# Optimization experiments

Hardware: AMD Instinct MI355X
Metric: run time of the kernel (lower is better)

The kernel has to match this reference:

```python
import jax, jax.numpy as jnp
import numpy as np

V = 50257   # vocab size (output_size / num_words)
H = 500     # hidden_size
S = 256     # source sequence length
MAXLEN = 64 # greedy decode steps
SOS = 1


def _gru_scan(xs, Wih, Whh, bih, bhh, reverse=False):
    """Run a GRU over xs: (S, Din) -> (outputs (S,H), final hidden (H,)).
    PyTorch gate order: r, z, n."""
    gx = xs @ Wih.T + bih  # (S, 3H), input-side gates precomputed
    Hh = Whh.shape[1]
    h0 = jnp.zeros((Hh,), dtype=xs.dtype)

    def step(h, g):
        gh = Whh @ h + bhh
        rx, zx, nx = jnp.split(g, 3)
        rh, zh, nh = jnp.split(gh, 3)
        r = jax.nn.sigmoid(rx + rh)
        z = jax.nn.sigmoid(zx + zh)
        n = jnp.tanh(nx + r * nh)
        h2 = (1.0 - z) * n + z * h
        return h2, h2

    hT, ys = jax.lax.scan(step, h0, gx, reverse=reverse)
    return ys, hT


def _gru_cell(x, h, Wih, Whh, bih, bhh):
    gx = Wih @ x + bih
    gh = Whh @ h + bhh
    rx, zx, nx = jnp.split(gx, 3)
    rh, zh, nh = jnp.split(gh, 3)
    r = jax.nn.sigmoid(rx + rh)
    z = jax.nn.sigmoid(zx + zh)
    n = jnp.tanh(nx + r * nh)
    return (1.0 - z) * n + z * h


def setup_inputs() -> dict:
    key = jax.random.key(0)
    ks = jax.random.split(key, 32)

    def p(k, shape):
        return jax.random.normal(k, shape, dtype=jnp.float32) * 0.05

    inp = {}
    inp["input_seq"] = jax.random.randint(ks[0], (S, 1), 0, V)
    inp["input_length"] = S
    inp["max_length"] = MAXLEN
    inp["emb"] = p(ks[1], (V, H))
    i = 2
    for name, din in [("enc0f", H), ("enc0b", H), ("enc1f", 2 * H), ("enc1b", 2 * H)]:
        inp[name + "_Wih"] = p(ks[i], (3 * H, din)); i += 1
        inp[name + "_Whh"] = p(ks[i], (3 * H, H)); i += 1
        inp[name + "_bih"] = p(ks[i], (3 * H,)); i += 1
        inp[name + "_bhh"] = p(ks[i], (3 * H,)); i += 1
    inp["dec_Wih"] = p(ks[i], (2, 3 * H, H)); i += 1
    inp["dec_Whh"] = p(ks[i], (2, 3 * H, H)); i += 1
    inp["dec_bih"] = p(ks[i], (2, 3 * H)); i += 1
    inp["dec_bhh"] = p(ks[i], (2, 3 * H)); i += 1
    inp["concat_W"] = p(ks[i], (H, 2 * H)); i += 1
    inp["concat_b"] = p(ks[i], (H,)); i += 1
    inp["out_W"] = p(ks[i], (V, H)); i += 1
    inp["out_b"] = p(ks[i], (V,)); i += 1
    return inp


def reference(input_seq, input_length, max_length, emb,
              enc0f_Wih, enc0f_Whh, enc0f_bih, enc0f_bhh,
              enc0b_Wih, enc0b_Whh, enc0b_bih, enc0b_bhh,
              enc1f_Wih, enc1f_Whh, enc1f_bih, enc1f_bhh,
              enc1b_Wih, enc1b_Whh, enc1b_bih, enc1b_bhh,
              dec_Wih, dec_Whh, dec_bih, dec_bhh,
              concat_W, concat_b, out_W, out_b):
    tokens = input_seq[:, 0]  # batch = 1
    ex = emb[tokens]          # (S, H) embedding lookup (dropout is eval no-op)

    # --- bidirectional 2-layer encoder GRU (full-length seq, batch=1) ---
    y0f, h0f = _gru_scan(ex, enc0f_Wih, enc0f_Whh, enc0f_bih, enc0f_bhh)
    y0b, h0b = _gru_scan(ex, enc0b_Wih, enc0b_Whh, enc0b_bih, enc0b_bhh, reverse=True)
    x1 = jnp.concatenate([y0f, y0b], axis=1)  # (S, 2H)
    y1f, _ = _gru_scan(x1, enc1f_Wih, enc1f_Whh, enc1f_bih, enc1f_bhh)
    y1b, _ = _gru_scan(x1, enc1b_Wih, enc1b_Whh, enc1b_bih, enc1b_bhh, reverse=True)
    enc_out = y1f + y1b  # (S, H): outputs[:, :H] + outputs[:, H:]

    # encoder_hidden[:n_layers] = [layer0_fwd, layer0_bwd] (PyTorch ordering)
    h_dec0 = jnp.stack([h0f, h0b])  # (2, H)

    def step(carry, _):
        h, tok = carry
        x = emb[tok]  # (H,)
        hs = []
        for l in range(2):  # 2 decoder GRU layers (dropout off in eval)
            hl = _gru_cell(x, h[l], dec_Wih[l], dec_Whh[l], dec_bih[l], dec_bhh[l])
            hs.append(hl)
            x = hl
        h2 = jnp.stack(hs)
        rnn = x  # (H,) top-layer output
        scores = enc_out @ rnn                 # dot attention: (S,)
        w = jax.nn.softmax(scores)
        ctx = w @ enc_out                      # (H,)
        c = jnp.tanh(concat_W @ jnp.concatenate([rnn, ctx]) + concat_b)
        probs = jax.nn.softmax(out_W @ c + out_b)  # (V,)
        tok2 = jnp.argmax(probs).astype(jnp.int32)
        return (h2, tok2), (tok2, probs)

    init = (h_dec0, jnp.asarray(SOS, dtype=jnp.int32))
    _, (all_tokens, all_probs) = jax.lax.scan(step, init, None, length=int(max_length))
    return all_tokens, all_probs
```

## Files before the change

kernel.cpp:

```cpp
#include <hip/hip_runtime.h>
#include <math.h>

typedef unsigned long long ull;

constexpr int H    = 500;
constexpr int H3   = 1500;
constexpr int SEQ  = 256;
constexpr int V    = 50257;
constexpr int TDEC = 64;
constexpr int NLT  = (V + 255) / 256;
constexpr int SB   = 50;
constexpr int UPB  = 10;
constexpr int NDB  = 256;
constexpr int VPB  = (V + NDB - 1) / NDB;

__device__ __forceinline__ float sigmoidf_(float x) { return 1.f / (1.f + expf(-x)); }

__device__ __forceinline__ float wred(float v) {
  #pragma unroll
  for (int off = 32; off > 0; off >>= 1) v += __shfl_down(v, off, 64);
  return v;
}

__device__ __forceinline__ float gload(const float* p) {
  return __hip_atomic_load((float*)p, __ATOMIC_RELAXED, __HIP_MEMORY_SCOPE_AGENT);
}
__device__ __forceinline__ void gstore(float* p, float v) {
  __hip_atomic_store(p, v, __ATOMIC_RELAXED, __HIP_MEMORY_SCOPE_AGENT);
}
__device__ __forceinline__ int gload_i(const int* p) {
  return __hip_atomic_load((int*)p, __ATOMIC_RELAXED, __HIP_MEMORY_SCOPE_AGENT);
}
__device__ __forceinline__ void gstore_i(int* p, int v) {
  __hip_atomic_store(p, v, __ATOMIC_RELAXED, __HIP_MEMORY_SCOPE_AGENT);
}
__device__ __forceinline__ ull gload64(const ull* p) {
  return __hip_atomic_load((ull*)p, __ATOMIC_RELAXED, __HIP_MEMORY_SCOPE_AGENT);
}
__device__ __forceinline__ void gstore64(ull* p, ull v) {
  __hip_atomic_store(p, v, __ATOMIC_RELAXED, __HIP_MEMORY_SCOPE_AGENT);
}

__device__ __forceinline__ void flagbar(int* flags, int nblk, int epoch, int blk) {
  __builtin_amdgcn_s_waitcnt(0);
  __syncthreads();
  if (threadIdx.x == 0) gstore_i(&flags[blk], epoch);
  if ((int)threadIdx.x < nblk)
    while (gload_i(&flags[threadIdx.x]) < epoch) {}
  __syncthreads();
}

__global__ void init_k(int* tok) {
  if (threadIdx.x == 0) tok[0] = 1;
}

__global__ void embed_k(const int* __restrict__ seq, const float* __restrict__ emb,
                        float* __restrict__ ex) {
  int t = blockIdx.x;
  int tok = seq[t];
  for (int i = threadIdx.x; i < H; i += blockDim.x)
    ex[(size_t)t * H + i] = emb[(size_t)tok * H + i];
}

__global__ __launch_bounds__(256) void gemm_nt(const float* __restrict__ X,
                                               const float* __restrict__ W,
                                               const float* __restrict__ bias,
                                               float* __restrict__ C,
                                               int M, int N, int K) {
  __shared__ float Xs[64][17];
  __shared__ float Ws[64][17];
  int bm = blockIdx.y * 64, bn = blockIdx.x * 64;
  int tid = threadIdx.x;
  int tx = tid % 16, ty = tid / 16;
  float acc[4][4] = {};
  for (int k0 = 0; k0 < K; k0 += 16) {
    for (int i = tid; i < 64 * 16; i += 256) {
      int m = i / 16, k = i % 16;
      int gm = bm + m, gk = k0 + k, gn = bn + m;
      Xs[m][k] = (gm < M && gk < K) ? X[(size_t)gm * K + gk] : 0.f;
      Ws[m][k] = (gn < N && gk < K) ? W[(size_t)gn * K + gk] : 0.f;
    }
    __syncthreads();
    #pragma unroll
    for (int k = 0; k < 16; ++k) {
      float xv[4], wv[4];
      #pragma unroll
      for (int i = 0; i < 4; ++i) xv[i] = Xs[ty * 4 + i][k];
      #pragma unroll
      for (int j = 0; j < 4; ++j) wv[j] = Ws[tx * 4 + j][k];
      #pragma unroll
      for (int i = 0; i < 4; ++i)
        #pragma unroll
        for (int j = 0; j < 4; ++j) acc[i][j] += xv[i] * wv[j];
    }
    __syncthreads();
  }
  for (int i = 0; i < 4; ++i) {
    int gm = bm + ty * 4 + i;
    if (gm >= M) continue;
    for (int j = 0; j < 4; ++j) {
      int gn = bn + tx * 4 + j;
      if (gn >= N) continue;
      C[(size_t)gm * N + gn] = acc[i][j] + bias[gn];
    }
  }
}

__global__ __launch_bounds__(512, 1) void gru_scan_tag(
    const float* __restrict__ gxF, const float* __restrict__ gxB,
    const float* __restrict__ WhhF, const float* __restrict__ WhhB,
    const float* __restrict__ bhhF, const float* __restrict__ bhhB,
    ull* __restrict__ tAF, ull* __restrict__ tBF,
    ull* __restrict__ tAB, ull* __restrict__ tBB,
    float* __restrict__ yF, float* __restrict__ yB, int ystride) {
  __shared__ float w_lds[30 * 500];
  __shared__ float gates[32];
  __shared__ float h_lds[512];
  int dir = blockIdx.x / SB;
  int bu  = blockIdx.x % SB;
  int u0  = bu * UPB;
  const float* gx  = dir ? gxB : gxF;
  const float* Whh = dir ? WhhB : WhhF;
  const float* bhh = dir ? bhhB : bhhF;
  ull* tagA = dir ? tAB : tAF;
  ull* tagB = dir ? tBB : tBF;
  float* y  = dir ? yB : yF;
  int tid = threadIdx.x, lane = tid & 63, wid = tid >> 6;

  for (int idx = tid; idx < 30 * 500; idx += 512) {
    int r = idx / 500, k = idx - r * 500;
    int g = r / UPB, lu = r - g * UPB;
    w_lds[idx] = Whh[(size_t)(g * 500 + u0 + lu) * 500 + k];
  }
  int u = u0 + tid;
  float br = 0.f, bz = 0.f, bn = 0.f;
  if (tid < UPB) { br = bhh[u]; bz = bhh[500 + u]; bn = bhh[1000 + u]; }
  h_lds[tid] = 0.f;
  __syncthreads();

  for (int t = 0; t < SEQ; ++t) {
    ull* wout = (t & 1) ? tagA : tagB;
    ull* win  = (t & 1) ? tagB : tagA;
    int teff = dir ? (SEQ - 1 - t) : t;

    float gxr = 0.f, gxz = 0.f, gxn = 0.f;
    if (tid < UPB) {
      const float* g = gx + (size_t)teff * H3;
      gxr = g[u]; gxz = g[500 + u]; gxn = g[1000 + u];
    }

    if (t > 0 && wid == 0) {
      ull v[8];
      for (;;) {
        bool ok = true;
        #pragma unroll
        for (int j = 0; j < 8; ++j) {
          int k = lane + 64 * j;
          if (k < 500) {
            v[j] = gload64(&win[k]);
            if ((unsigned)(v[j] >> 32) != (unsigned)t) ok = false;
          }
        }
        if (ok) break;
        __builtin_amdgcn_s_sleep(1);
      }
      #pragma unroll
      for (int j = 0; j < 8; ++j) {
        int k = lane + 64 * j;
        if (k < 500) h_lds[k] = __uint_as_float((unsigned)v[j]);
      }
    }
    __syncthreads();

    float hreg[8];
    #pragma unroll
    for (int j = 0; j < 8; ++j) {
      int k = lane + 64 * j;
      hreg[j] = (k < 500) ? h_lds[k] : 0.f;
    }
    for (int r = wid; r < 30; r += 8) {
      const float* wr = &w_lds[r * 500];
      float acc = 0.f;
      #pragma unroll
      for (int j = 0; j < 8; ++j) {
        int k = lane + 64 * j;
        if (k < 500) acc += wr[k] * hreg[j];
      }
      acc = wred(acc);
      if (lane == 0) gates[r] = acc;
    }
    __syncthreads();
    if (tid < UPB) {
      float hold = h_lds[u];
      float rr = sigmoidf_(gxr + gates[tid]           + br);
      float zz = sigmoidf_(gxz + gates[UPB + tid]     + bz);
      float nn = tanhf(    gxn + rr * (gates[2 * UPB + tid] + bn));
      float hp = (1.f - zz) * nn + zz * hold;
      ull pv = ((ull)(unsigned)(t + 1) << 32) | (ull)__float_as_uint(hp);
      gstore64(&wout[u], pv);
      y[(size_t)teff * ystride + u] = hp;
    }
  }
}

__global__ void unpack_k(const ull* __restrict__ ta, const ull* __restrict__ tb,
                         float* __restrict__ ha, float* __restrict__ hb_) {
  int i = threadIdx.x;
  if (i < 500) {
    ha[i]  = __uint_as_float((unsigned)ta[i]);
    hb_[i] = __uint_as_float((unsigned)tb[i]);
  }
}

__global__ void add_k(const float* __restrict__ a, const float* __restrict__ b,
                      float* __restrict__ c, int n) {
  int i = blockIdx.x * blockDim.x + threadIdx.x;
  if (i < n) c[i] = a[i] + b[i];
}

__device__ __forceinline__ void cell_unit(int u, int lane, const float* xf, const float* hf,
    const float* __restrict__ Wih, const float* __restrict__ Whh,
    const float* __restrict__ bih, const float* __restrict__ bhh, float* hout) {
  float g[6];
  #pragma unroll
  for (int kind = 0; kind < 6; ++kind) {
    const float* row = (kind < 3) ? (Wih + (size_t)(kind * 500 + u) * 500)
                                  : (Whh + (size_t)((kind - 3) * 500 + u) * 500);
    const float* vec = (kind < 3) ? xf : hf;
    float acc = 0.f;
    #pragma unroll
    for (int j = 0; j < 8; ++j) {
      int k = lane + 64 * j;
      if (k < 500) acc += row[k] * vec[k];
    }
    g[kind] = wred(acc);
  }
  if (lane == 0) {
    float r = sigmoidf_(g[0] + bih[u]        + g[3] + bhh[u]);
    float z = sigmoidf_(g[1] + bih[500 + u]  + g[4] + bhh[500 + u]);
    float n = tanhf(    g[2] + bih[1000 + u] + r * (g[5] + bhh[1000 + u]));
    gstore(&hout[u], (1.f - z) * n + z * hf[u]);
  }
}

__global__ __launch_bounds__(512, 1) void dec_step_v4(
    int* __restrict__ tokp, const float* __restrict__ emb,
    const float* __restrict__ h0in, float* __restrict__ h0out,
    const float* __restrict__ h1in, float* __restrict__ h1out,
    const float* __restrict__ dWih, const float* __restrict__ dWhh,
    const float* __restrict__ dbih, const float* __restrict__ dbhh,
    const float* __restrict__ enc_out, const float* __restrict__ cW,
    const float* __restrict__ cb,
    const float* __restrict__ outW, const float* __restrict__ outb,
    float* __restrict__ scores, float* __restrict__ ctx, float* __restrict__ cvec,
    float* __restrict__ logits, float* __restrict__ pm, float* __restrict__ ps,
    int* __restrict__ pix, float* __restrict__ stats,
    float* __restrict__ out_tokens, float* __restrict__ out_probs,
    int* dflags, int* dcnt, int st) {
  __shared__ float4 v4[250];
  __shared__ float red[256], sc[256];
  __shared__ float wm[8], wsum[8]; __shared__ int wix[8];
  __shared__ float mm[256], ms[256]; __shared__ int mi[256];
  __shared__ int lastf;
  float* xf = (float*)v4;
  float* hf = xf + 500;
  int tid = threadIdx.x, lane = tid & 63, wid = tid >> 6, blk = blockIdx.x;
  int ep = st * 5;

  if (st > 0) {
    float mM = stats[2 * (st - 1)], iS = stats[2 * (st - 1) + 1];
    int base = blk * VPB;
    for (int r = tid; r < VPB; r += 512) {
      int v = base + r;
      if (v < V) out_probs[(size_t)(st - 1) * V + v] = expf(logits[v] - mM) * iS;
    }
  }

  if (blk < 63) {
    int u = blk * 8 + wid;
    int tk = tokp[0];
    for (int i = tid; i < 500; i += 512) {
      xf[i] = emb[(size_t)tk * 500 + i];
      hf[i] = h0in[i];
    }
    __syncthreads();
    if (u < 500) cell_unit(u, lane, xf, hf, dWih, dWhh, dbih, dbhh, h0out);
    flagbar(dflags, 63, ep + 1, blk);

    for (int i = tid; i < 500; i += 512) {
      xf[i] = gload(&h0out[i]);
      hf[i] = h1in[i];
    }
    __syncthreads();
    if (u < 500) cell_unit(u, lane, xf, hf,
        dWih + 750000, dWhh + 750000, dbih + 1500, dbhh + 1500, h1out);
    flagbar(dflags, 63, ep + 2, blk);

    for (int i = tid; i < 500; i += 512) xf[i] = gload(&h1out[i]);
    __syncthreads();
    if (blk < 32) {
      int s = blk * 8 + wid;
      const float* row = enc_out + (size_t)s * 500;
      float acc = 0.f;
      #pragma unroll
      for (int j = 0; j < 8; ++j) {
        int k = lane + 64 * j;
        if (k < 500) acc += row[k] * xf[k];
      }
      acc = wred(acc);
      if (lane == 0) gstore(&scores[s], acc);
    }
    flagbar(dflags, 63, ep + 3, blk);

    {
      float myv = 0.f;
      if (tid < 256) { myv = gload(&scores[tid]); red[tid] = myv; }
      __syncthreads();
      for (int s = 128; s > 0; s >>= 1) {
        if (tid < s) red[tid] = fmaxf(red[tid], red[tid + s]);
        __syncthreads();
      }
      float m = red[0]; __syncthreads();
      float e = 0.f;
      if (tid < 256) { e = expf(myv - m); red[tid] = e; }
      __syncthreads();
      for (int s = 128; s > 0; s >>= 1) {
        if (tid < s) red[tid] += red[tid + s];
        __syncthreads();
      }
      float inv = 1.f / red[0]; __syncthreads();
      if (tid < 256) sc[tid] = e * inv;
      __syncthreads();
      int j = blk * 8 + wid;
      if (j < 500) {
        float acc = 0.f;
        #pragma unroll
        for (int q = 0; q < 4; ++q) {
          int s = lane + 64 * q;
          acc += sc[s] * enc_out[(size_t)s * 500 + j];
        }
        acc = wred(acc);
        if (lane == 0) gstore(&ctx[j], acc);
      }
    }
    flagbar(dflags, 63, ep + 4, blk);

    for (int i = tid; i < 500; i += 512) {
      xf[i] = gload(&h1out[i]);
      hf[i] = gload(&ctx[i]);
    }
    __syncthreads();
    {
      int i = blk * 8 + wid;
      if (i < 500) {
        const float* row = cW + (size_t)i * 1000;
        float acc = 0.f;
        #pragma unroll
        for (int j = 0; j < 16; ++j) {
          int k = lane + 64 * j;
          if (k < 1000) acc += row[k] * xf[k];
        }
        acc = wred(acc);
        if (lane == 0) gstore(&cvec[i], tanhf(acc + cb[i]));
      }
    }
  }

  __builtin_amdgcn_s_waitcnt(0);
  __syncthreads();
  if (blk < 63 && tid == 0) gstore_i(&dflags[blk], ep + 5);
  if (tid < 63) {
    while (gload_i(&dflags[tid]) < ep + 5) __builtin_amdgcn_s_sleep(2);
  }
  __syncthreads();

  for (int i = tid; i < 500; i += 512) xf[i] = gload(&cvec[i]);
  __syncthreads();
  const float4* c4 = v4;
  {
    int lstart = wid * 25, lend = (wid + 1) * 25; if (lend > VPB) lend = VPB;
    int r0 = blk * VPB + lstart, r1 = blk * VPB + lend; if (r1 > V) r1 = V;
    float m = -1e30f, ssum = 0.f; int ix = V;
    for (int rb = r0; rb < r1; rb += 4) {
      int nr = r1 - rb; if (nr > 4) nr = 4;
      float a[4] = {0.f, 0.f, 0.f, 0.f};
      #pragma unroll
      for (int q = 0; q < 2; ++q) {
        int k4 = lane + 64 * q;
        if (k4 < 125) {
          float4 cc = c4[k4];
          #pragma unroll
          for (int rr = 0; rr < 4; ++rr) {
            if (rr < nr) {
              float4 w4 = ((const float4*)(outW + (size_t)(rb + rr) * 500))[k4];
              a[rr] += w4.x * cc.x + w4.y * cc.y + w4.z * cc.z + w4.w * cc.w;
            }
          }
        }
      }
      #pragma unroll
      for (int rr = 0; rr < 4; ++rr) {
        if (rr < nr) {
          float l = wred(a[rr]);
          if (lane == 0) {
            l += outb[rb + rr];
            logits[rb + rr] = l;
            if (l > m) { ssum = ssum * expf(m - l) + 1.f; m = l; ix = rb + rr; }
            else       { ssum += expf(l - m); }
          }
        }
      }
    }
    if (lane == 0) { wm[wid] = m; wsum[wid] = ssum; wix[wid] = ix; }
  }
  __syncthreads();
  if (tid == 0) {
    float M = wm[0], S = wsum[0]; int I = wix[0];
    for (int w = 1; w < 8; ++w) {
      if (wm[w] > M) { S = S * expf(M - wm[w]) + wsum[w]; M = wm[w]; I = wix[w]; }
      else           { S += wsum[w] * expf(wm[w] - M); }
    }
    gstore(&pm[blk], M); gstore(&ps[blk], S); gstore_i(&pix[blk], I);
    __builtin_amdgcn_s_waitcnt(0);
    int prev = __hip_atomic_fetch_add(&dcnt[st], 1, __ATOMIC_RELAXED,
                                      __HIP_MEMORY_SCOPE_AGENT);
    lastf = (prev == NDB - 1) ? 1 : 0;
  }
  __syncthreads();

  if (lastf) {
    if (tid < 256) { mm[tid] = gload(&pm[tid]); ms[tid] = gload(&ps[tid]); mi[tid] = gload_i(&pix[tid]); }
    __syncthreads();
    for (int s = 128; s > 0; s >>= 1) {
      if (tid < s) {
        float ma = mm[tid], mb = mm[tid + s];
        float sa = ms[tid], sb = ms[tid + s];
        int ia = mi[tid], ib = mi[tid + s];
        if (mb > ma || (mb == ma && ib < ia)) {
          ms[tid] = sa * expf(ma - mb) + sb; mm[tid] = mb; mi[tid] = ib;
        } else {
          ms[tid] = sa + sb * expf(mb - ma);
        }
      }
      __syncthreads();
    }
    if (tid == 0) {
      tokp[0] = mi[0];
      out_tokens[st] = (float)mi[0];
      stats[2 * st] = mm[0];
      stats[2 * st + 1] = 1.f / ms[0];
    }
  }
}

__global__ __launch_bounds__(256) void probs_k(const float* __restrict__ logits,
    const float* __restrict__ stats, float* __restrict__ out_probs) {
  int v = blockIdx.x * 256 + threadIdx.x;
  if (v < V) out_probs[v] = expf(logits[v] - stats[0]) * stats[1];
}

extern "C" void kernel_launch(void* const* d_in, const int* in_sizes, int n_in,
                              void* d_out, int out_size, void* d_ws, size_t ws_size,
                              hipStream_t stream) {
  const int*   seq   = (const int*)d_in[0];
  const float* emb   = (const float*)d_in[3];
  const float* e0f_Wih = (const float*)d_in[4];
  const float* e0f_Whh = (const float*)d_in[5];
  const float* e0f_bih = (const float*)d_in[6];
  const float* e0f_bhh = (const float*)d_in[7];
  const float* e0b_Wih = (const float*)d_in[8];
  const float* e0b_Whh = (const float*)d_in[9];
  const float* e0b_bih = (const float*)d_in[10];
  const float* e0b_bhh = (const float*)d_in[11];
  const float* e1f_Wih = (const float*)d_in[12];
  const float* e1f_Whh = (const float*)d_in[13];
  const float* e1f_bih = (const float*)d_in[14];
  const float* e1f_bhh = (const float*)d_in[15];
  const float* e1b_Wih = (const float*)d_in[16];
  const float* e1b_Whh = (const float*)d_in[17];
  const float* e1b_bih = (const float*)d_in[18];
  const float* e1b_bhh = (const float*)d_in[19];
  const float* dWih = (const float*)d_in[20];
  const float* dWhh = (const float*)d_in[21];
  const float* dbih = (const float*)d_in[22];
  const float* dbhh = (const float*)d_in[23];
  const float* cW   = (const float*)d_in[24];
  const float* cb   = (const float*)d_in[25];
  const float* outW = (const float*)d_in[26];
  const float* outb = (const float*)d_in[27];

  float* w = (float*)d_ws;
  float* ex      = w;
  float* x1      = ex + 128000;
  float* gxf     = x1 + 256000;
  float* gxb     = gxf + 384000;
  float* y1f     = gxb + 384000;
  float* y1b     = y1f + 128000;
  float* enc_out = y1b + 128000;
  float* hb      = enc_out + 128000;
  float* hL0FA = hb;          float* hL0BA = hb + 512;
  float* dsc0   = hb + 1024;
  float* dsc1   = dsc0 + 512;
  float* scores = dsc1 + 512;
  float* ctx    = scores + 512;
  float* cvec   = ctx + 512;
  float* logits = cvec + 512;
  float* pm     = logits + 50432;
  float* ps     = pm + 256;
  float* stats  = ps + 256;
  int*   pix    = (int*)(stats + 192);
  int*   tokp   = pix + 256;
  int*   bar    = tokp + 64;
  int*   dflags = bar;
  int*   dcnt   = bar + 64;
  ull*   htag   = (ull*)(bar + 128);
  ull* tL0F_A = htag;        ull* tL0F_B = htag + 512;
  ull* tL0B_A = htag + 1024; ull* tL0B_B = htag + 1536;
  ull* tL1F_A = htag + 2048; ull* tL1F_B = htag + 2560;
  ull* tL1B_A = htag + 3072; ull* tL1B_B = htag + 3584;

  float* outf = (float*)d_out;

  hipMemsetAsync(bar, 0, 128 * sizeof(int) + 4096 * sizeof(ull), stream);

  init_k<<<1, 64, 0, stream>>>(tokp);
  embed_k<<<SEQ, 128, 0, stream>>>(seq, emb, ex);

  gemm_nt<<<dim3(24, 4), 256, 0, stream>>>(ex, e0f_Wih, e0f_bih, gxf, SEQ, H3, H);
  gemm_nt<<<dim3(24, 4), 256, 0, stream>>>(ex, e0b_Wih, e0b_bih, gxb, SEQ, H3, H);
  gru_scan_tag<<<2 * SB, 512, 0, stream>>>(gxf, gxb, e0f_Whh, e0b_Whh,
      e0f_bhh, e0b_bhh, tL0F_A, tL0F_B, tL0B_A, tL0B_B, x1, x1 + 500, 1000);
  unpack_k<<<1, 512, 0, stream>>>(tL0F_A, tL0B_A, hL0FA, hL0BA);

  gemm_nt<<<dim3(24, 4), 256, 0, stream>>>(x1, e1f_Wih, e1f_bih, gxf, SEQ, H3, 2 * H);
  gemm_nt<<<dim3(24, 4), 256, 0, stream>>>(x1, e1b_Wih, e1b_bih, gxb, SEQ, H3, 2 * H);
  gru_scan_tag<<<2 * SB, 512, 0, stream>>>(gxf, gxb, e1f_Whh, e1b_Whh,
      e1f_bhh, e1b_bhh, tL1F_A, tL1F_B, tL1B_A, tL1B_B, y1f, y1b, 500);
  add_k<<<(SEQ * H + 255) / 256, 256, 0, stream>>>(y1f, y1b, enc_out, SEQ * H);

  float* h0c = hL0FA; float* h0a = dsc0;
  float* h1c = hL0BA; float* h1a = dsc1;
  for (int st = 0; st < TDEC; ++st) {
    dec_step_v4<<<NDB, 512, 0, stream>>>(tokp, emb, h0c, h0a, h1c, h1a,
        dWih, dWhh, dbih, dbhh, enc_out, cW, cb, outW, outb,
        scores, ctx, cvec, logits, pm, ps, pix, stats,
        outf, outf + TDEC, dflags, dcnt, st);
    float* t0 = h0c; h0c = h0a; h0a = t0;
    float* t1 = h1c; h1c = h1a; h1a = t1;
  }
  probs_k<<<NLT, 256, 0, stream>>>(logits, stats + 2 * (TDEC - 1),
      outf + TDEC + (size_t)(TDEC - 1) * V);
}
```

Baseline: 6.869 ms.

## Replace decoder flag barriers with tagged-value dataflow polling and double-buffered logits

Drops the per-phase all-block flag barriers in the decoder step. Each producer now writes a 64-bit value carrying a step tag, and consumers poll only the tags of the data they need. Logits are double-buffered so that the worker blocks can defer writing the previous step's probabilities until after their critical-path work. This is meant to cut barrier latency on the serial decode chain, in exchange for more polling traffic on the tag arrays and more complex memory-ordering assumptions.

```diff
diff --git a/kernel.cpp b/kernel.cpp
--- a/kernel.cpp
+++ b/kernel.cpp
@@ -31,9 +31,6 @@
 __device__ __forceinline__ int gload_i(const int* p) {
   return __hip_atomic_load((int*)p, __ATOMIC_RELAXED, __HIP_MEMORY_SCOPE_AGENT);
 }
-__device__ __forceinline__ void gstore_i(int* p, int v) {
-  __hip_atomic_store(p, v, __ATOMIC_RELAXED, __HIP_MEMORY_SCOPE_AGENT);
-}
 __device__ __forceinline__ ull gload64(const ull* p) {
   return __hip_atomic_load((ull*)p, __ATOMIC_RELAXED, __HIP_MEMORY_SCOPE_AGENT);
 }
@@ -41,12 +38,69 @@
   __hip_atomic_store(p, v, __ATOMIC_RELAXED, __HIP_MEMORY_SCOPE_AGENT);
 }
 
-__device__ __forceinline__ void flagbar(int* flags, int nblk, int epoch, int blk) {
-  __builtin_amdgcn_s_waitcnt(0);
+template<int N>
+__device__ __forceinline__ void poll_tags(const ull* tags, unsigned want,
+                                          float* dst, int tid) {
+  constexpr int NW = (N + 63) / 64;
+  if (tid < 64) {
+    ull v[NW];
+    bool ok;
+    do {
+      ok = true;
+      #pragma unroll
+      for (int j = 0; j < NW; ++j) {
+        int k = tid + (j << 6);
+        if (k < N) {
+          v[j] = gload64(&tags[k]);
+          if ((unsigned)(v[j] >> 32) != want) ok = false;
+        }
+      }
+      if (!ok) __builtin_amdgcn_s_sleep(1);
+    } while (!ok);
+    #pragma unroll
+    for (int j = 0; j < NW; ++j) {
+      int k = tid + (j << 6);
+      if (k < N) dst[k] = __uint_as_float((unsigned)v[j]);
+    }
+  }
   __syncthreads();
-  if (threadIdx.x == 0) gstore_i(&flags[blk], epoch);
-  if ((int)threadIdx.x < nblk)
-    while (gload_i(&flags[threadIdx.x]) < epoch) {}
+}
+
+__device__ __forceinline__ void poll2_tags(const ull* tA, float* dA,
+                                           const ull* tB, float* dB,
+                                           unsigned want, int tid) {
+  if (tid < 64) {
+    ull va[8], vb[4];
+    bool ok;
+    do {
+      ok = true;
+      #pragma unroll
+      for (int j = 0; j < 8; ++j) {
+        int k = tid + (j << 6);
+        if (k < 500) {
+          va[j] = gload64(&tA[k]);
+          if ((unsigned)(va[j] >> 32) != want) ok = false;
+        }
+      }
+      #pragma unroll
+      for (int j = 0; j < 4; ++j) {
+        int k = tid + (j << 6);
+        vb[j] = gload64(&tB[k]);
+        if ((unsigned)(vb[j] >> 32) != want) ok = false;
+      }
+      if (!ok) __builtin_amdgcn_s_sleep(1);
+    } while (!ok);
+    #pragma unroll
+    for (int j = 0; j < 8; ++j) {
+      int k = tid + (j << 6);
+      if (k < 500) dA[k] = __uint_as_float((unsigned)va[j]);
+    }
+    #pragma unroll
+    for (int j = 0; j < 4; ++j) {
+      int k = tid + (j << 6);
+      dB[k] = __uint_as_float((unsigned)vb[j]);
+    }
+  }
   __syncthreads();
 }
 
@@ -218,9 +272,11 @@
   if (i < n) c[i] = a[i] + b[i];
 }
 
-__device__ __forceinline__ void cell_unit(int u, int lane, const float* xf, const float* hf,
+__device__ __forceinline__ void cell_unit_pub(int u, int lane,
+    const float* xf, const float* hf,
     const float* __restrict__ Wih, const float* __restrict__ Whh,
-    const float* __restrict__ bih, const float* __restrict__ bhh, float* hout) {
+    const float* __restrict__ bih, const float* __restrict__ bhh,
+    float* hplain, ull* htag, unsigned want) {
   float g[6];
   #pragma unroll
   for (int kind = 0; kind < 6; ++kind) {
@@ -239,11 +295,13 @@
     float r = sigmoidf_(g[0] + bih[u]        + g[3] + bhh[u]);
     float z = sigmoidf_(g[1] + bih[500 + u]  + g[4] + bhh[500 + u]);
     float n = tanhf(    g[2] + bih[1000 + u] + r * (g[5] + bhh[1000 + u]));
-    gstore(&hout[u], (1.f - z) * n + z * hf[u]);
-  }
-}
-
-__global__ __launch_bounds__(512, 1) void dec_step_v4(
+    float hv = (1.f - z) * n + z * hf[u];
+    hplain[u] = hv;
+    gstore64(&htag[u], ((ull)want << 32) | (ull)__float_as_uint(hv));
+  }
+}
+
+__global__ __launch_bounds__(512, 1) void dec_step_v5(
     int* __restrict__ tokp, const float* __restrict__ emb,
     const float* __restrict__ h0in, float* __restrict__ h0out,
     const float* __restrict__ h1in, float* __restrict__ h1out,
@@ -252,12 +310,14 @@
     const float* __restrict__ enc_out, const float* __restrict__ cW,
     const float* __restrict__ cb,
     const float* __restrict__ outW, const float* __restrict__ outb,
-    float* __restrict__ scores, float* __restrict__ ctx, float* __restrict__ cvec,
-    float* __restrict__ logits, float* __restrict__ pm, float* __restrict__ ps,
-    int* __restrict__ pix, float* __restrict__ stats,
-    float* __restrict__ out_tokens, float* __restrict__ out_probs,
-    int* dflags, int* dcnt, int st) {
+    ull* __restrict__ th0, ull* __restrict__ th1, ull* __restrict__ tsc,
+    ull* __restrict__ tctx, ull* __restrict__ tcvec,
+    float* __restrict__ lg_w, const float* __restrict__ lg_r,
+    float* __restrict__ pm, float* __restrict__ ps, int* __restrict__ pix,
+    float* __restrict__ stats, float* __restrict__ out_tokens,
+    float* __restrict__ out_probs, int* __restrict__ dcnt, int st) {
   __shared__ float4 v4[250];
+  __shared__ float hfull[512];
   __shared__ float red[256], sc[256];
   __shared__ float wm[8], wsum[8]; __shared__ int wix[8];
   __shared__ float mm[256], ms[256]; __shared__ int mi[256];
@@ -265,56 +325,58 @@
   float* xf = (float*)v4;
   float* hf = xf + 500;
   int tid = threadIdx.x, lane = tid & 63, wid = tid >> 6, blk = blockIdx.x;
-  int ep = st * 5;
-
-  if (st > 0) {
+  unsigned want = (unsigned)(st + 1);
+  bool worker = blk < 63;
+  int u = blk * 8 + wid;
+
+  if (!worker && st > 0) {
     float mM = stats[2 * (st - 1)], iS = stats[2 * (st - 1) + 1];
     int base = blk * VPB;
     for (int r = tid; r < VPB; r += 512) {
       int v = base + r;
-      if (v < V) out_probs[(size_t)(st - 1) * V + v] = expf(logits[v] - mM) * iS;
-    }
-  }
-
-  if (blk < 63) {
-    int u = blk * 8 + wid;
+      if (v < V) out_probs[(size_t)(st - 1) * V + v] = expf(lg_r[v] - mM) * iS;
+    }
+  }
+
+  if (worker) {
     int tk = tokp[0];
     for (int i = tid; i < 500; i += 512) {
       xf[i] = emb[(size_t)tk * 500 + i];
       hf[i] = h0in[i];
     }
     __syncthreads();
-    if (u < 500) cell_unit(u, lane, xf, hf, dWih, dWhh, dbih, dbhh, h0out);
-    flagbar(dflags, 63, ep + 1, blk);
-
-    for (int i = tid; i < 500; i += 512) {
-      xf[i] = gload(&h0out[i]);
-      hf[i] = h1in[i];
-    }
-    __syncthreads();
-    if (u < 500) cell_unit(u, lane, xf, hf,
-        dWih + 750000, dWhh + 750000, dbih + 1500, dbhh + 1500, h1out);
-    flagbar(dflags, 63, ep + 2, blk);
-
-    for (int i = tid; i < 500; i += 512) xf[i] = gload(&h1out[i]);
-    __syncthreads();
+    if (u < 500) cell_unit_pub(u, lane, xf, hf, dWih, dWhh, dbih, dbhh,
+                               h0out, th0, want);
+    __syncthreads();
+
+    if (tid >= 64) for (int i = tid - 64; i < 500; i += 448) hf[i] = h1in[i];
+    poll_tags<500>(th0, want, xf, tid);
+    if (u < 500) cell_unit_pub(u, lane, xf, hf,
+        dWih + 750000, dWhh + 750000, dbih + 1500, dbhh + 1500,
+        h1out, th1, want);
+    __syncthreads();
+
     if (blk < 32) {
+      poll_tags<500>(th1, want, hfull, tid);
       int s = blk * 8 + wid;
       const float* row = enc_out + (size_t)s * 500;
       float acc = 0.f;
       #pragma unroll
       for (int j = 0; j < 8; ++j) {
         int k = lane + 64 * j;
-        if (k < 500) acc += row[k] * xf[k];
+        if (k < 500) acc += row[k] * hfull[k];
       }
       acc = wred(acc);
-      if (lane == 0) gstore(&scores[s], acc);
-    }
-    flagbar(dflags, 63, ep + 3, blk);
+      if (lane == 0)
+        gstore64(&tsc[s], ((ull)want << 32) | (ull)__float_as_uint(acc));
+      poll_tags<256>(tsc, want, sc, tid);
+    } else {
+      poll2_tags(th1, hfull, tsc, sc, want, tid);
+    }
 
     {
-      float myv = 0.f;
-      if (tid < 256) { myv = gload(&scores[tid]); red[tid] = myv; }
+      float myv = (tid < 256) ? sc[tid] : 0.f;
+      if (tid < 256) red[tid] = myv;
       __syncthreads();
       for (int s = 128; s > 0; s >>= 1) {
         if (tid < s) red[tid] = fmaxf(red[tid], red[tid + s]);
@@ -340,16 +402,13 @@
           acc += sc[s] * enc_out[(size_t)s * 500 + j];
         }
         acc = wred(acc);
-        if (lane == 0) gstore(&ctx[j], acc);
-      }
-    }
-    flagbar(dflags, 63, ep + 4, blk);
-
-    for (int i = tid; i < 500; i += 512) {
-      xf[i] = gload(&h1out[i]);
-      hf[i] = gload(&ctx[i]);
-    }
-    __syncthreads();
+        if (lane == 0)
+          gstore64(&tctx[j], ((ull)want << 32) | (ull)__float_as_uint(acc));
+      }
+    }
+
+    if (tid >= 64) for (int i = tid - 64; i < 500; i += 448) xf[i] = hfull[i];
+    poll_tags<500>(tctx, want, hf, tid);
     {
       int i = blk * 8 + wid;
       if (i < 500) {
@@ -361,21 +420,16 @@
           if (k < 1000) acc += row[k] * xf[k];
         }
         acc = wred(acc);
-        if (lane == 0) gstore(&cvec[i], tanhf(acc + cb[i]));
-      }
-    }
-  }
-
-  __builtin_amdgcn_s_waitcnt(0);
-  __syncthreads();
-  if (blk < 63 && tid == 0) gstore_i(&dflags[blk], ep + 5);
-  if (tid < 63) {
-    while (gload_i(&dflags[tid]) < ep + 5) __builtin_amdgcn_s_sleep(2);
-  }
-  __syncthreads();
-
-  for (int i = tid; i < 500; i += 512) xf[i] = gload(&cvec[i]);
-  __syncthreads();
+        if (lane == 0) {
+          float cv = tanhf(acc + cb[i]);
+          gstore64(&tcvec[i], ((ull)want << 32) | (ull)__float_as_uint(cv));
+        }
+      }
+    }
+    __syncthreads();
+  }
+
+  poll_tags<500>(tcvec, want, xf, tid);
   const float4* c4 = v4;
   {
     int lstart = wid * 25, lend = (wid + 1) * 25; if (lend > VPB) lend = VPB;
@@ -404,7 +458,7 @@
           float l = wred(a[rr]);
           if (lane == 0) {
             l += outb[rb + rr];
-            logits[rb + rr] = l;
+            lg_w[rb + rr] = l;
             if (l > m) { ssum = ssum * expf(m - l) + 1.f; m = l; ix = rb + rr; }
             else       { ssum += expf(l - m); }
           }
@@ -420,7 +474,8 @@
       if (wm[w] > M) { S = S * expf(M - wm[w]) + wsum[w]; M = wm[w]; I = wix[w]; }
       else           { S += wsum[w] * expf(wm[w] - M); }
     }
-    gstore(&pm[blk], M); gstore(&ps[blk], S); gstore_i(&pix[blk], I);
+    gstore(&pm[blk], M); gstore(&ps[blk], S);
+    __hip_atomic_store(&pix[blk], I, __ATOMIC_RELAXED, __HIP_MEMORY_SCOPE_AGENT);
     __builtin_amdgcn_s_waitcnt(0);
     int prev = __hip_atomic_fetch_add(&dcnt[st], 1, __ATOMIC_RELAXED,
                                       __HIP_MEMORY_SCOPE_AGENT);
@@ -449,6 +504,15 @@
       out_tokens[st] = (float)mi[0];
       stats[2 * st] = mm[0];
       stats[2 * st + 1] = 1.f / ms[0];
+    }
+  }
+
+  if (worker && st > 0) {
+    float mM = stats[2 * (st - 1)], iS = stats[2 * (st - 1) + 1];
+    int base = blk * VPB;
+    for (int r = tid; r < VPB; r += 512) {
+      int v = base + r;
+      if (v < V) out_probs[(size_t)(st - 1) * V + v] = expf(lg_r[v] - mM) * iS;
     }
   }
 }
@@ -497,31 +561,31 @@
   float* y1f     = gxb + 384000;
   float* y1b     = y1f + 128000;
   float* enc_out = y1b + 128000;
-  float* hb      = enc_out + 128000;
-  float* hL0FA = hb;          float* hL0BA = hb + 512;
-  float* dsc0   = hb + 1024;
-  float* dsc1   = dsc0 + 512;
-  float* scores = dsc1 + 512;
-  float* ctx    = scores + 512;
-  float* cvec   = ctx + 512;
-  float* logits = cvec + 512;
-  float* pm     = logits + 50432;
-  float* ps     = pm + 256;
-  float* stats  = ps + 256;
-  int*   pix    = (int*)(stats + 192);
-  int*   tokp   = pix + 256;
-  int*   bar    = tokp + 64;
-  int*   dflags = bar;
-  int*   dcnt   = bar + 64;
-  ull*   htag   = (ull*)(bar + 128);
+  float* hL0FA   = enc_out + 128000;
+  float* hL0BA   = hL0FA + 512;
+  float* dsc0    = hL0BA + 512;
+  float* dsc1    = dsc0 + 512;
+  float* lg0     = dsc1 + 512;
+  float* lg1     = lg0 + 50432;
+  float* pm      = lg1 + 50432;
+  float* ps      = pm + 256;
+  float* stats   = ps + 256;
+  int*   pix     = (int*)(stats + 192);
+  int*   tokp    = pix + 256;
+  int*   dcnt    = tokp + 64;
+  ull*   htag    = (ull*)(dcnt + 64);
   ull* tL0F_A = htag;        ull* tL0F_B = htag + 512;
   ull* tL0B_A = htag + 1024; ull* tL0B_B = htag + 1536;
   ull* tL1F_A = htag + 2048; ull* tL1F_B = htag + 2560;
   ull* tL1B_A = htag + 3072; ull* tL1B_B = htag + 3584;
+  ull*   dtag    = htag + 4096;
+  ull* th0   = dtag;        ull* th1  = dtag + 512;
+  ull* tsc   = dtag + 1024; ull* tctx = dtag + 1280;
+  ull* tcvec = dtag + 1792;
 
   float* outf = (float*)d_out;
 
-  hipMemsetAsync(bar, 0, 128 * sizeof(int) + 4096 * sizeof(ull), stream);
+  hipMemsetAsync(dcnt, 0, 64 * sizeof(int) + 6400 * sizeof(ull), stream);
 
   init_k<<<1, 64, 0, stream>>>(tokp);
   embed_k<<<SEQ, 128, 0, stream>>>(seq, emb, ex);
@@ -541,13 +605,15 @@
   float* h0c = hL0FA; float* h0a = dsc0;
   float* h1c = hL0BA; float* h1a = dsc1;
   for (int st = 0; st < TDEC; ++st) {
-    dec_step_v4<<<NDB, 512, 0, stream>>>(tokp, emb, h0c, h0a, h1c, h1a,
+    float* lg_w = (st & 1) ? lg1 : lg0;
+    float* lg_r = (st & 1) ? lg0 : lg1;
+    dec_step_v5<<<NDB, 512, 0, stream>>>(tokp, emb, h0c, h0a, h1c, h1a,
         dWih, dWhh, dbih, dbhh, enc_out, cW, cb, outW, outb,
-        scores, ctx, cvec, logits, pm, ps, pix, stats,
-        outf, outf + TDEC, dflags, dcnt, st);
+        th0, th1, tsc, tctx, tcvec, lg_w, lg_r,
+        pm, ps, pix, stats, outf, outf + TDEC, dcnt, st);
     float* t0 = h0c; h0c = h0a; h0a = t0;
     float* t1 = h1c; h1c = h1a; h1a = t1;
   }
-  probs_k<<<NLT, 256, 0, stream>>>(logits, stats + 2 * (TDEC - 1),
-      outf + TDEC + (size_t)(TDEC - 1) * V);
-}
+  probs_k<<<NLT, 256, 0, stream>>>(((TDEC - 1) & 1) ? lg1 : lg0,
+      stats + 2 * (TDEC - 1), outf + TDEC + (size_t)(TDEC - 1) * V);
+}
```

Measured after the change: 6.294 ms. 1.09x faster.
